# Optimization experiments

Measured on AMD Instinct MI355X. Metric: run time of the kernel, lower is better.

The kernel has to match this reference:

```python
import jax, jax.numpy as jnp
import numpy as np

DIM, H, HD = 512, 8, 64
N_BANK = 4096
EPS = 1e-5


def layernorm(x, g, b):
    m = jnp.mean(x, axis=-1, keepdims=True)
    v = jnp.mean(jnp.square(x - m), axis=-1, keepdims=True)
    return (x - m) * jax.lax.rsqrt(v + EPS) * g + b


def setup_inputs() -> dict:
    key = jax.random.key(0)
    ks = jax.random.split(key, 8)
    # xavier_uniform bound for square (512,512) linears
    bound = float(np.sqrt(6.0 / (DIM + DIM)))
    inp = {
        "x_q": jax.random.normal(ks[0], (32, 128, DIM), jnp.float32),
        "x_k": jax.random.normal(ks[1], (N_BANK, DIM), jnp.float32),
        "x_v": jax.random.normal(ks[2], (N_BANK, DIM), jnp.float32),
        "Wq": jax.random.uniform(ks[3], (DIM, DIM), jnp.float32, -bound, bound),
        "Wk": jax.random.uniform(ks[4], (DIM, DIM), jnp.float32, -bound, bound),
        "Wv": jax.random.uniform(ks[5], (DIM, DIM), jnp.float32, -bound, bound),
        "Wproj": jax.random.uniform(ks[6], (DIM, DIM), jnp.float32, -bound, bound),
        "qn_g": jnp.ones((HD,), jnp.float32),
        "qn_b": jnp.zeros((HD,), jnp.float32),
        "kn_g": jnp.ones((HD,), jnp.float32),
        "kn_b": jnp.zeros((HD,), jnp.float32),
        "n_g": jnp.ones((DIM,), jnp.float32),
        "n_b": jnp.zeros((DIM,), jnp.float32),
    }
    return inp


def reference(x_q, x_k, x_v, Wq, Wk, Wv, Wproj, qn_g, qn_b, kn_g, kn_b, n_g, n_b):
    B, S, D = x_q.shape
    N = x_k.shape[0]
    scale = HD ** (-0.5)
    # Linear layers (torch: y = x @ W.T)
    q = jnp.einsum('bsd,od->bso', x_q, Wq).reshape(B, S, H, HD).transpose(0, 2, 1, 3)  # (B,H,S,hd)
    k = jnp.einsum('nd,od->no', x_k, Wk).reshape(N, H, HD).transpose(1, 0, 2)          # (H,N,hd)
    v = jnp.einsum('nd,od->no', x_v, Wv).reshape(N, H, HD).transpose(1, 0, 2)          # (H,N,hd)
    # per-head qk layernorm
    q = layernorm(q, qn_g, qn_b) * scale
    k = layernorm(k, kn_g, kn_b)
    # cross-attention to shared bank (K/V have no batch dim)
    attn = jnp.einsum('bhsd,hnd->bhsn', q, k)          # (B,H,S,N)
    attn = jax.nn.softmax(attn, axis=-1)
    x = jnp.einsum('bhsn,hnd->bhsd', attn, v)          # (B,H,S,hd)
    x = x.transpose(0, 2, 1, 3).reshape(B, S, D)
    x = layernorm(x, n_g, n_b)
    x = jnp.einsum('bsd,od->bso', x, Wproj)
    return x
```

## Files before the change

### kernel.cpp

```cpp
#include <hip/hip_runtime.h>
#include <hip/hip_bf16.h>
#include <math.h>

#define DIM 512
#define NHEAD 8
#define HD 64
#define NBANK 4096
#define NQROWS 4096
#define EPS 1e-5f
#define QSCALE 0.18033688011f
#define PART_ELEMS (NQROWS * DIM)

typedef __attribute__((ext_vector_type(4))) float floatx4;
typedef __attribute__((ext_vector_type(8))) short short8;

#if defined(__has_builtin)
#if __has_builtin(__builtin_amdgcn_exp2f)
#define EXP2(x) __builtin_amdgcn_exp2f(x)
#endif
#endif
#ifndef EXP2
#define EXP2(x) __expf((x) * 0.69314718056f)
#endif

__device__ __forceinline__ unsigned short f2bf(float f) {
    unsigned int u = __float_as_uint(f);
    u += 0x7fffu + ((u >> 16) & 1u);
    return (unsigned short)(u >> 16);
}
__device__ __forceinline__ float bf2f(unsigned short h) {
    return __uint_as_float(((unsigned int)h) << 16);
}
__device__ __forceinline__ unsigned int pk2(float a, float b) {
    union { __hip_bfloat162 h; unsigned int u; } cvt;
    cvt.h = __float22bfloat162_rn(make_float2(a, b));
    return cvt.u;
}
__device__ __forceinline__ void dma16(const void* gsrc, void* ldst) {
    __builtin_amdgcn_global_load_lds(
        (const __attribute__((address_space(1))) unsigned int*)gsrc,
        (__attribute__((address_space(3))) unsigned int*)ldst, 16, 0, 0);
}

__global__ __launch_bounds__(256) void cvt_kernel(
    const float* __restrict__ Wq, const float* __restrict__ Wk,
    const float* __restrict__ Wv, const float* __restrict__ Wp,
    const float* __restrict__ xq, const float* __restrict__ xk,
    const float* __restrict__ xv,
    unsigned short* __restrict__ Wb, unsigned short* __restrict__ Xb)
{
    const int y = blockIdx.y;
    const float* src;
    unsigned short* dst;
    if (y < 4) {
        if (blockIdx.x >= 128) return;
        src = (y == 0) ? Wq : (y == 1) ? Wk : (y == 2) ? Wv : Wp;
        dst = Wb + (size_t)y * DIM * DIM;
    } else {
        src = (y == 4) ? xq : (y == 5) ? xk : xv;
        dst = Xb + (size_t)(y - 4) * NQROWS * DIM;
    }
    const int i = (blockIdx.x * 256 + threadIdx.x) * 8;
    const int row = i >> 9, kpos = i & 511;
    const int kt = kpos >> 6, seg = (kpos >> 3) & 7;
    const float4 a0 = *(const float4*)(src + i);
    const float4 a1 = *(const float4*)(src + i + 4);
    union { short8 v; unsigned int u[4]; } t;
    t.u[0] = pk2(a0.x, a0.y); t.u[1] = pk2(a0.z, a0.w);
    t.u[2] = pk2(a1.x, a1.y); t.u[3] = pk2(a1.z, a1.w);
    *(short8*)(dst + (size_t)row * 512 + kt * 64 + ((seg ^ (row & 7)) << 3)) = t.v;
}

__global__ __launch_bounds__(256) void qkv_kernel(
    const unsigned short* __restrict__ Xb, const unsigned short* __restrict__ Wb,
    const float* __restrict__ qg, const float* __restrict__ qbeta,
    const float* __restrict__ kg, const float* __restrict__ kbeta,
    unsigned short* __restrict__ Qb, unsigned short* __restrict__ Kb,
    unsigned short* __restrict__ VTb)
{
    __shared__ short8 smem[3072];
    const int tid  = threadIdx.x;
    const int w    = tid >> 6, lane = tid & 63, m = lane & 15, q = lane >> 4;
    const int wr   = w & 1, wc = w >> 1;
    const int row0 = blockIdx.x * 64;
    const int mat  = blockIdx.y >> 2;
    const int col0 = (blockIdx.y & 3) * 128;
    const unsigned short* Xm = Xb + (size_t)mat * NQROWS * DIM;
    const unsigned short* Wm = Wb + (size_t)mat * DIM * DIM;

    const int it0 = tid, it1 = tid + 256;
    const unsigned short* asrc0 = Xm + (size_t)(row0 + (it0 >> 3)) * DIM + (it0 & 7) * 8;
    const unsigned short* asrc1 = Xm + (size_t)(row0 + (it1 >> 3)) * DIM + (it1 & 7) * 8;
    const unsigned short* bsrc[4];
    #pragma unroll
    for (int j = 0; j < 4; ++j) {
        const int item = j * 256 + tid;
        bsrc[j] = Wm + (size_t)(col0 + (item >> 3)) * DIM + (item & 7) * 8;
    }

    floatx4 acc[2][4];
    #pragma unroll
    for (int mt = 0; mt < 2; ++mt)
        #pragma unroll
        for (int nt = 0; nt < 4; ++nt) acc[mt][nt] = (floatx4){0.f, 0.f, 0.f, 0.f};

    {
        short8* as = smem; short8* bs = smem + 512;
        dma16(asrc0, as + w * 64);
        dma16(asrc1, as + 256 + w * 64);
        #pragma unroll
        for (int j = 0; j < 4; ++j)
            dma16(bsrc[j], bs + j * 256 + w * 64);
    }
    __syncthreads();

    for (int kt = 0; kt < 8; ++kt) {
        short8* as = smem + (kt & 1) * 1536;
        short8* bs = as + 512;
        if (kt < 7) {
            short8* asn = smem + ((kt + 1) & 1) * 1536;
            short8* bsn = asn + 512;
            const int o = (kt + 1) * 64;
            dma16(asrc0 + o, asn + w * 64);
            dma16(asrc1 + o, asn + 256 + w * 64);
            #pragma unroll
            for (int j = 0; j < 4; ++j)
                dma16(bsrc[j] + o, bsn + j * 256 + w * 64);
        }
        #pragma unroll
        for (int s = 0; s < 2; ++s) {
            short8 af[2], bfr[4];
            #pragma unroll
            for (int mt = 0; mt < 2; ++mt)
                af[mt] = as[(wr * 32 + mt * 16 + m) * 8 + ((s * 4 + q) ^ (m & 7))];
            #pragma unroll
            for (int nt = 0; nt < 4; ++nt)
                bfr[nt] = bs[(wc * 64 + nt * 16 + m) * 8 + ((s * 4 + q) ^ (m & 7))];
            #pragma unroll
            for (int mt = 0; mt < 2; ++mt)
                #pragma unroll
                for (int nt = 0; nt < 4; ++nt)
                    acc[mt][nt] = __builtin_amdgcn_mfma_f32_16x16x32_bf16(af[mt], bfr[nt], acc[mt][nt], 0, 0, 0);
        }
        __syncthreads();
    }

    if (mat < 2) {
        const float* g = (mat == 0) ? qg : kg;
        const float* be = (mat == 0) ? qbeta : kbeta;
        unsigned short* Y = (mat == 0) ? Qb : Kb;
        float gv[4], bv[4];
        #pragma unroll
        for (int nt = 0; nt < 4; ++nt) { gv[nt] = g[nt * 16 + m]; bv[nt] = be[nt * 16 + m]; }
        #pragma unroll
        for (int mt = 0; mt < 2; ++mt) {
            #pragma unroll
            for (int r = 0; r < 4; ++r) {
                float s = 0.f, sq = 0.f;
                #pragma unroll
                for (int nt = 0; nt < 4; ++nt) { const float v = acc[mt][nt][r]; s += v; sq += v * v; }
                s  += __shfl_xor(s, 1);  s  += __shfl_xor(s, 2);  s  += __shfl_xor(s, 4);  s  += __shfl_xor(s, 8);
                sq += __shfl_xor(sq, 1); sq += __shfl_xor(sq, 2); sq += __shfl_xor(sq, 4); sq += __shfl_xor(sq, 8);
                const float mean = s * (1.f / HD);
                const float var  = sq * (1.f / HD) - mean * mean;
                const float rr   = rsqrtf(var + EPS);
                const int grow = row0 + wr * 32 + mt * 16 + q * 4 + r;
                #pragma unroll
                for (int nt = 0; nt < 4; ++nt) {
                    float v = (acc[mt][nt][r] - mean) * rr * gv[nt] + bv[nt];
                    if (mat == 0) v *= QSCALE;
                    const int col = col0 + wc * 64 + nt * 16 + m;
                    int scol = col;
                    if (mat == 1) {
                        const int o = col & 63, sg2 = o >> 3;
                        scol = (col & ~63) | (((sg2 ^ (grow & 7)) << 3) | (o & 7));
                    }
                    Y[(size_t)grow * DIM + scol] = f2bf(v);
                }
            }
        }
    } else {
        unsigned short* vt = (unsigned short*)smem;
        __syncthreads();
        #pragma unroll
        for (int mt = 0; mt < 2; ++mt)
            #pragma unroll
            for (int nt = 0; nt < 4; ++nt) {
                const int c  = wc * 64 + nt * 16 + m;
                const int rw = wr * 32 + mt * 16 + q * 4;
                *(unsigned int*)(vt + c * 88 + rw)     = pk2(acc[mt][nt][0], acc[mt][nt][1]);
                *(unsigned int*)(vt + c * 88 + rw + 2) = pk2(acc[mt][nt][2], acc[mt][nt][3]);
            }
        __syncthreads();
        #pragma unroll
        for (int p = 0; p < 4; ++p) {
            const int idx = p * 256 + tid;
            const int c = idx >> 3, g = idx & 7;
            const int dglob = col0 + c, hh = dglob >> 6, dl = dglob & 63;
            const int pos = (g >> 2) * 32 + (g & 3) * 4;
            union { short8 v; ushort4 h4[2]; } tv;
            tv.h4[0] = *(const ushort4*)(vt + c * 88 + pos);
            tv.h4[1] = *(const ushort4*)(vt + c * 88 + pos + 16);
            *(short8*)(VTb + ((size_t)(hh * 64 + blockIdx.x) * 512
                              + dl * 8 + (g ^ (dl & 7))) * 8) = tv.v;
        }
    }
}

__global__ __launch_bounds__(256) void attn_kernel(
    const unsigned short* __restrict__ Qb, const unsigned short* __restrict__ Kb,
    const unsigned short* __restrict__ VTb, unsigned short* __restrict__ AOp,
    float* __restrict__ sums)
{
    __shared__ short8 smem[2048];
    const int tid  = threadIdx.x;
    const int w    = tid >> 6;
    const int lane = tid & 63;
    const int m    = lane & 15;
    const int Qd   = lane >> 4;
    const int h    = blockIdx.x & 7;
    const int qgi  = blockIdx.x >> 3;
    const int row0 = qgi * 128;
    const int part = blockIdx.y;
    const int c0   = part * 16;

    const int it0 = tid, it1 = tid + 256;
    const unsigned short* ksrc0 = Kb + (size_t)(it0 >> 3) * DIM + h * HD + (it0 & 7) * 8;
    const unsigned short* ksrc1 = Kb + (size_t)(it1 >> 3) * DIM + h * HD + (it1 & 7) * 8;
    const unsigned short* vbase = VTb + (size_t)h * 64 * 512 * 8;

    short8 qf[2][2];
    #pragma unroll
    for (int mt = 0; mt < 2; ++mt)
        #pragma unroll
        for (int s = 0; s < 2; ++s)
            qf[mt][s] = *(const short8*)(Qb + (size_t)(row0 + w * 32 + mt * 16 + m) * DIM
                                         + h * HD + s * 32 + Qd * 8);

    floatx4 of[4][2];
    floatx4 sacc[2];
    #pragma unroll
    for (int t = 0; t < 4; ++t)
        #pragma unroll
        for (int mt = 0; mt < 2; ++mt) of[t][mt] = (floatx4){0.f, 0.f, 0.f, 0.f};
    #pragma unroll
    for (int mt = 0; mt < 2; ++mt) sacc[mt] = (floatx4){0.f, 0.f, 0.f, 0.f};
    union { short8 v; unsigned int u[4]; } onesu;
    #pragma unroll
    for (int u = 0; u < 4; ++u) onesu.u[u] = 0x3F803F80u;

    {
        short8* ks = smem; short8* vts = smem + 512;
        dma16(ksrc0 + (size_t)c0 * 64 * DIM, ks + w * 64);
        dma16(ksrc1 + (size_t)c0 * 64 * DIM, ks + 256 + w * 64);
        dma16(vbase + ((size_t)c0 * 512 + it0) * 8, vts + w * 64);
        dma16(vbase + ((size_t)c0 * 512 + it1) * 8, vts + 256 + w * 64);
    }
    __syncthreads();

    for (int c = 0; c < 16; ++c) {
        short8* ks  = smem + (c & 1) * 1024;
        short8* vts = ks + 512;
        if (c < 15) {
            short8* ksn  = smem + ((c + 1) & 1) * 1024;
            short8* vtsn = ksn + 512;
            const size_t nc = c0 + c + 1;
            dma16(ksrc0 + nc * 64 * DIM, ksn + w * 64);
            dma16(ksrc1 + nc * 64 * DIM, ksn + 256 + w * 64);
            dma16(vbase + (nc * 512 + it0) * 8, vtsn + w * 64);
            dma16(vbase + (nc * 512 + it1) * 8, vtsn + 256 + w * 64);
        }

        floatx4 st[4][2];
        #pragma unroll
        for (int t = 0; t < 4; ++t)
            #pragma unroll
            for (int mt = 0; mt < 2; ++mt) st[t][mt] = (floatx4){0.f, 0.f, 0.f, 0.f};
        #pragma unroll
        for (int s = 0; s < 2; ++s)
            #pragma unroll
            for (int t = 0; t < 4; ++t) {
                const short8 kf = ks[(t * 16 + m) * 8 + ((s * 4 + Qd) ^ (m & 7))];
                #pragma unroll
                for (int mt = 0; mt < 2; ++mt)
                    st[t][mt] = __builtin_amdgcn_mfma_f32_16x16x32_bf16(kf, qf[mt][s], st[t][mt], 0, 0, 0);
            }

        union { short8 v; unsigned int u[4]; } pf[2][2];
        #pragma unroll
        for (int mt = 0; mt < 2; ++mt)
            #pragma unroll
            for (int s2 = 0; s2 < 2; ++s2)
                #pragma unroll
                for (int u = 0; u < 4; ++u) {
                    const int t = s2 * 2 + (u >> 1), r = (u & 1) * 2;
                    pf[mt][s2].u[u] = pk2(EXP2(st[t][mt][r]), EXP2(st[t][mt][r + 1]));
                }

        #pragma unroll
        for (int mt = 0; mt < 2; ++mt)
            #pragma unroll
            for (int s2 = 0; s2 < 2; ++s2)
                sacc[mt] = __builtin_amdgcn_mfma_f32_16x16x32_bf16(onesu.v, pf[mt][s2].v, sacc[mt], 0, 0, 0);

        #pragma unroll
        for (int s2 = 0; s2 < 2; ++s2)
            #pragma unroll
            for (int t2 = 0; t2 < 4; ++t2) {
                const short8 vf = vts[(t2 * 16 + m) * 8 + ((s2 * 4 + Qd) ^ (m & 7))];
                #pragma unroll
                for (int mt = 0; mt < 2; ++mt)
                    of[t2][mt] = __builtin_amdgcn_mfma_f32_16x16x32_bf16(vf, pf[mt][s2].v, of[t2][mt], 0, 0, 0);
            }
        __syncthreads();
    }

    if (Qd == 0) {
        #pragma unroll
        for (int mt = 0; mt < 2; ++mt)
            sums[((size_t)part * NQROWS + row0 + w * 32 + mt * 16 + m) * NHEAD + h] = sacc[mt][0];
    }

    unsigned int* ob = (unsigned int*)smem;
    #pragma unroll
    for (int t2 = 0; t2 < 4; ++t2)
        #pragma unroll
        for (int mt = 0; mt < 2; ++mt) {
            const int qq  = w * 32 + mt * 16 + m;
            const int blk = t2 * 2 + (Qd >> 1);
            const int sub = (Qd & 1) * 2;
            const int bs  = (blk ^ (qq & 7)) * 4;
            ob[qq * 32 + bs + sub]     = pk2(of[t2][mt][0], of[t2][mt][1]);
            ob[qq * 32 + bs + sub + 1] = pk2(of[t2][mt][2], of[t2][mt][3]);
        }
    __syncthreads();
    #pragma unroll
    for (int pp = 0; pp < 4; ++pp) {
        const int idx = tid + pp * 256;
        const int qq = idx >> 3, sg = idx & 7;
        *(short8*)(AOp + (size_t)part * PART_ELEMS + (size_t)(row0 + qq) * DIM + h * HD + sg * 8) =
            smem[qq * 8 + (sg ^ (qq & 7))];
    }
}

__global__ __launch_bounds__(256) void combine_kernel(
    const unsigned short* __restrict__ AOp, const float* __restrict__ sums,
    const float* __restrict__ g, const float* __restrict__ be,
    unsigned short* __restrict__ AO)
{
    __shared__ float rs[256], rq[256], sm[2], sr[2];
    const int tid  = threadIdx.x;
    const int half = tid >> 7;
    const int row  = blockIdx.x * 2 + half;
    const int t    = tid & 127;
    const int h    = t >> 4;

    float stot = 0.f;
    #pragma unroll
    for (int p = 0; p < 4; ++p)
        stot += sums[((size_t)p * NQROWS + row) * NHEAD + h];

    float o[4] = {0.f, 0.f, 0.f, 0.f};
    #pragma unroll
    for (int p = 0; p < 4; ++p) {
        const ushort4 u = *(const ushort4*)(AOp + (size_t)p * PART_ELEMS + (size_t)row * DIM + t * 4);
        o[0] += bf2f(u.x); o[1] += bf2f(u.y); o[2] += bf2f(u.z); o[3] += bf2f(u.w);
    }
    const float inv = 1.0f / stot;
    const float v0 = o[0] * inv, v1 = o[1] * inv, v2 = o[2] * inv, v3 = o[3] * inv;

    rs[tid] = v0 + v1 + v2 + v3;
    rq[tid] = v0 * v0 + v1 * v1 + v2 * v2 + v3 * v3;
    __syncthreads();
    #pragma unroll
    for (int off = 64; off > 0; off >>= 1) {
        if (t < off) { rs[tid] += rs[tid + off]; rq[tid] += rq[tid + off]; }
        __syncthreads();
    }
    if (t == 0) {
        const float mean = rs[tid] * (1.f / DIM);
        const float var  = rq[tid] * (1.f / DIM) - mean * mean;
        sm[half] = mean;
        sr[half] = rsqrtf(var + EPS);
    }
    __syncthreads();

    const float mean = sm[half], rstd = sr[half];
    const float4 g4 = *(const float4*)(g + t * 4);
    const float4 b4 = *(const float4*)(be + t * 4);
    uint2 packed;
    packed.x = pk2((v0 - mean) * rstd * g4.x + b4.x, (v1 - mean) * rstd * g4.y + b4.y);
    packed.y = pk2((v2 - mean) * rstd * g4.z + b4.z, (v3 - mean) * rstd * g4.w + b4.w);
    const int kt = t >> 4, seg = (t >> 1) & 7, jof = (t & 1) * 4;
    *(uint2*)(AO + (size_t)row * DIM + kt * 64 + ((seg ^ (row & 7)) << 3) + jof) = packed;
}

__global__ __launch_bounds__(256) void final_kernel(
    const unsigned short* __restrict__ AO, const unsigned short* __restrict__ Wpb,
    float* __restrict__ out)
{
    __shared__ short8 fs[2048];
    const int tid  = threadIdx.x;
    const int w    = tid >> 6, lane = tid & 63, m = lane & 15, q = lane >> 4;
    const int row0 = blockIdx.x * 64;
    const int col0 = blockIdx.y * 64;

    const int it0 = tid, it1 = tid + 256;
    const unsigned short* asrc0 = AO  + (size_t)(row0 + (it0 >> 3)) * DIM + (it0 & 7) * 8;
    const unsigned short* asrc1 = AO  + (size_t)(row0 + (it1 >> 3)) * DIM + (it1 & 7) * 8;
    const unsigned short* wsrc0 = Wpb + (size_t)(col0 + (it0 >> 3)) * DIM + (it0 & 7) * 8;
    const unsigned short* wsrc1 = Wpb + (size_t)(col0 + (it1 >> 3)) * DIM + (it1 & 7) * 8;

    floatx4 acc[4];
    #pragma unroll
    for (int mt = 0; mt < 4; ++mt) acc[mt] = (floatx4){0.f, 0.f, 0.f, 0.f};

    {
        dma16(asrc0, fs + w * 64);
        dma16(asrc1, fs + 256 + w * 64);
        dma16(wsrc0, fs + 512 + w * 64);
        dma16(wsrc1, fs + 768 + w * 64);
    }
    __syncthreads();

    for (int kt = 0; kt < 8; ++kt) {
        short8* buf  = fs + (kt & 1) * 1024;
        if (kt < 7) {
            short8* bufn = fs + ((kt + 1) & 1) * 1024;
            const int o = (kt + 1) * 64;
            dma16(asrc0 + o, bufn + w * 64);
            dma16(asrc1 + o, bufn + 256 + w * 64);
            dma16(wsrc0 + o, bufn + 512 + w * 64);
            dma16(wsrc1 + o, bufn + 768 + w * 64);
        }
        #pragma unroll
        for (int s = 0; s < 2; ++s) {
            short8 af[4];
            #pragma unroll
            for (int mt = 0; mt < 4; ++mt)
                af[mt] = buf[(mt * 16 + m) * 8 + ((s * 4 + q) ^ (m & 7))];
            const short8 bfr = buf[512 + (w * 16 + m) * 8 + ((s * 4 + q) ^ (m & 7))];
            #pragma unroll
            for (int mt = 0; mt < 4; ++mt)
                acc[mt] = __builtin_amdgcn_mfma_f32_16x16x32_bf16(af[mt], bfr, acc[mt], 0, 0, 0);
        }
        __syncthreads();
    }

    #pragma unroll
    for (int mt = 0; mt < 4; ++mt)
        #pragma unroll
        for (int r = 0; r < 4; ++r)
            out[(size_t)(row0 + mt * 16 + q * 4 + r) * DIM + col0 + w * 16 + m] = acc[mt][r];
}

extern "C" void kernel_launch(void* const* d_in, const int* in_sizes, int n_in,
                              void* d_out, int out_size, void* d_ws, size_t ws_size,
                              hipStream_t stream)
{
    const float* x_q = (const float*)d_in[0];
    const float* x_k = (const float*)d_in[1];
    const float* x_v = (const float*)d_in[2];
    const float* Wq  = (const float*)d_in[3];
    const float* Wk  = (const float*)d_in[4];
    const float* Wv  = (const float*)d_in[5];
    const float* Wp  = (const float*)d_in[6];
    const float* qg  = (const float*)d_in[7];
    const float* qb  = (const float*)d_in[8];
    const float* kg  = (const float*)d_in[9];
    const float* kb  = (const float*)d_in[10];
    const float* ng  = (const float*)d_in[11];
    const float* nb  = (const float*)d_in[12];
    float* out = (float*)d_out;

    unsigned short* Qb   = (unsigned short*)d_ws;
    unsigned short* Kb   = Qb  + (size_t)NQROWS * DIM;
    unsigned short* VTb  = Kb  + (size_t)NBANK * DIM;
    unsigned short* AOp  = VTb + (size_t)NBANK * DIM;
    float*          sums = (float*)(AOp + (size_t)4 * PART_ELEMS);
    unsigned short* Wb   = (unsigned short*)(sums + (size_t)4 * NQROWS * NHEAD);
    unsigned short* Xb   = AOp;
    unsigned short* AO   = Qb;

    cvt_kernel<<<dim3(1024, 7), 256, 0, stream>>>(Wq, Wk, Wv, Wp, x_q, x_k, x_v, Wb, Xb);
    qkv_kernel<<<dim3(64, 12), 256, 0, stream>>>(Xb, Wb, qg, qb, kg, kb, Qb, Kb, VTb);
    attn_kernel<<<dim3(256, 4), 256, 0, stream>>>(Qb, Kb, VTb, AOp, sums);
    combine_kernel<<<NQROWS / 2, 256, 0, stream>>>(AOp, sums, ng, nb, AO);
    final_kernel<<<dim3(64, 8), 256, 0, stream>>>(AO, Wb + (size_t)3 * DIM * DIM, out);
}
```

Measured before the change: 172.7 us.

## Triple-buffer K/V and GEMM tiles with vmcnt waits; sum softmax in VALU

```diff
diff --git a/kernel.cpp b/kernel.cpp
--- a/kernel.cpp
+++ b/kernel.cpp
@@ -20,7 +20,7 @@
 #endif
 #endif
 #ifndef EXP2
-#define EXP2(x) __expf((x) * 0.69314718056f)
+#define EXP2(x) exp2f(x)
 #endif
 
 __device__ __forceinline__ unsigned short f2bf(float f) {
@@ -212,7 +212,7 @@
     const unsigned short* __restrict__ VTb, unsigned short* __restrict__ AOp,
     float* __restrict__ sums)
 {
-    __shared__ short8 smem[2048];
+    __shared__ short8 smem[3072];
     const int tid  = threadIdx.x;
     const int w    = tid >> 6;
     const int lane = tid & 63;
@@ -238,16 +238,12 @@
                                          + h * HD + s * 32 + Qd * 8);
 
     floatx4 of[4][2];
-    floatx4 sacc[2];
+    float sump[2] = {0.f, 0.f};
     #pragma unroll
     for (int t = 0; t < 4; ++t)
         #pragma unroll
         for (int mt = 0; mt < 2; ++mt) of[t][mt] = (floatx4){0.f, 0.f, 0.f, 0.f};
-    #pragma unroll
-    for (int mt = 0; mt < 2; ++mt) sacc[mt] = (floatx4){0.f, 0.f, 0.f, 0.f};
-    union { short8 v; unsigned int u[4]; } onesu;
-    #pragma unroll
-    for (int u = 0; u < 4; ++u) onesu.u[u] = 0x3F803F80u;
+    const floatx4 fz = (floatx4){0.f, 0.f, 0.f, 0.f};
 
     {
         short8* ks = smem; short8* vts = smem + 512;
@@ -255,16 +251,27 @@
         dma16(ksrc1 + (size_t)c0 * 64 * DIM, ks + 256 + w * 64);
         dma16(vbase + ((size_t)c0 * 512 + it0) * 8, vts + w * 64);
         dma16(vbase + ((size_t)c0 * 512 + it1) * 8, vts + 256 + w * 64);
-    }
-    __syncthreads();
-
+        short8* ks1 = smem + 1024; short8* vts1 = ks1 + 512;
+        const size_t c1 = (size_t)c0 + 1;
+        dma16(ksrc0 + c1 * 64 * DIM, ks1 + w * 64);
+        dma16(ksrc1 + c1 * 64 * DIM, ks1 + 256 + w * 64);
+        dma16(vbase + (c1 * 512 + it0) * 8, vts1 + w * 64);
+        dma16(vbase + (c1 * 512 + it1) * 8, vts1 + 256 + w * 64);
+    }
+
+    int cb = 0, nb = 2;
     for (int c = 0; c < 16; ++c) {
-        short8* ks  = smem + (c & 1) * 1024;
+        if (c < 15) asm volatile("s_waitcnt vmcnt(4)" ::: "memory");
+        else        asm volatile("s_waitcnt vmcnt(0)" ::: "memory");
+        __builtin_amdgcn_s_barrier();
+        __builtin_amdgcn_sched_barrier(0);
+
+        short8* ks  = smem + cb * 1024;
         short8* vts = ks + 512;
-        if (c < 15) {
-            short8* ksn  = smem + ((c + 1) & 1) * 1024;
+        if (c < 14) {
+            short8* ksn  = smem + nb * 1024;
             short8* vtsn = ksn + 512;
-            const size_t nc = c0 + c + 1;
+            const size_t nc = (size_t)(c0 + c + 2);
             dma16(ksrc0 + nc * 64 * DIM, ksn + w * 64);
             dma16(ksrc1 + nc * 64 * DIM, ksn + 256 + w * 64);
             dma16(vbase + (nc * 512 + it0) * 8, vtsn + w * 64);
@@ -273,18 +280,19 @@
 
         floatx4 st[4][2];
         #pragma unroll
-        for (int t = 0; t < 4; ++t)
-            #pragma unroll
-            for (int mt = 0; mt < 2; ++mt) st[t][mt] = (floatx4){0.f, 0.f, 0.f, 0.f};
-        #pragma unroll
-        for (int s = 0; s < 2; ++s)
-            #pragma unroll
-            for (int t = 0; t < 4; ++t) {
-                const short8 kf = ks[(t * 16 + m) * 8 + ((s * 4 + Qd) ^ (m & 7))];
-                #pragma unroll
-                for (int mt = 0; mt < 2; ++mt)
-                    st[t][mt] = __builtin_amdgcn_mfma_f32_16x16x32_bf16(kf, qf[mt][s], st[t][mt], 0, 0, 0);
-            }
+        for (int t = 0; t < 4; ++t) {
+            const short8 kf = ks[(t * 16 + m) * 8 + (Qd ^ (m & 7))];
+            #pragma unroll
+            for (int mt = 0; mt < 2; ++mt)
+                st[t][mt] = __builtin_amdgcn_mfma_f32_16x16x32_bf16(kf, qf[mt][0], fz, 0, 0, 0);
+        }
+        #pragma unroll
+        for (int t = 0; t < 4; ++t) {
+            const short8 kf = ks[(t * 16 + m) * 8 + ((4 + Qd) ^ (m & 7))];
+            #pragma unroll
+            for (int mt = 0; mt < 2; ++mt)
+                st[t][mt] = __builtin_amdgcn_mfma_f32_16x16x32_bf16(kf, qf[mt][1], st[t][mt], 0, 0, 0);
+        }
 
         union { short8 v; unsigned int u[4]; } pf[2][2];
         #pragma unroll
@@ -294,14 +302,12 @@
                 #pragma unroll
                 for (int u = 0; u < 4; ++u) {
                     const int t = s2 * 2 + (u >> 1), r = (u & 1) * 2;
-                    pf[mt][s2].u[u] = pk2(EXP2(st[t][mt][r]), EXP2(st[t][mt][r + 1]));
+                    const float e0 = EXP2(st[t][mt][r]);
+                    const float e1 = EXP2(st[t][mt][r + 1]);
+                    sump[mt] += e0;
+                    sump[mt] += e1;
+                    pf[mt][s2].u[u] = pk2(e0, e1);
                 }
-
-        #pragma unroll
-        for (int mt = 0; mt < 2; ++mt)
-            #pragma unroll
-            for (int s2 = 0; s2 < 2; ++s2)
-                sacc[mt] = __builtin_amdgcn_mfma_f32_16x16x32_bf16(onesu.v, pf[mt][s2].v, sacc[mt], 0, 0, 0);
 
         #pragma unroll
         for (int s2 = 0; s2 < 2; ++s2)
@@ -312,13 +318,23 @@
                 for (int mt = 0; mt < 2; ++mt)
                     of[t2][mt] = __builtin_amdgcn_mfma_f32_16x16x32_bf16(vf, pf[mt][s2].v, of[t2][mt], 0, 0, 0);
             }
-        __syncthreads();
-    }
-
+
+        cb = (cb == 2) ? 0 : cb + 1;
+        nb = (nb == 2) ? 0 : nb + 1;
+    }
+    __syncthreads();
+
+    #pragma unroll
+    for (int mt = 0; mt < 2; ++mt) {
+        float s = sump[mt];
+        s += __shfl_xor(s, 16);
+        s += __shfl_xor(s, 32);
+        sump[mt] = s;
+    }
     if (Qd == 0) {
         #pragma unroll
         for (int mt = 0; mt < 2; ++mt)
-            sums[((size_t)part * NQROWS + row0 + w * 32 + mt * 16 + m) * NHEAD + h] = sacc[mt][0];
+            sums[((size_t)part * NQROWS + row0 + w * 32 + mt * 16 + m) * NHEAD + h] = sump[mt];
     }
 
     unsigned int* ob = (unsigned int*)smem;
@@ -399,7 +415,7 @@
     const unsigned short* __restrict__ AO, const unsigned short* __restrict__ Wpb,
     float* __restrict__ out)
 {
-    __shared__ short8 fs[2048];
+    __shared__ short8 fs[3072];
     const int tid  = threadIdx.x;
     const int w    = tid >> 6, lane = tid & 63, m = lane & 15, q = lane >> 4;
     const int row0 = blockIdx.x * 64;
@@ -420,14 +436,23 @@
         dma16(asrc1, fs + 256 + w * 64);
         dma16(wsrc0, fs + 512 + w * 64);
         dma16(wsrc1, fs + 768 + w * 64);
-    }
-    __syncthreads();
-
+        dma16(asrc0 + 64, fs + 1024 + w * 64);
+        dma16(asrc1 + 64, fs + 1024 + 256 + w * 64);
+        dma16(wsrc0 + 64, fs + 1024 + 512 + w * 64);
+        dma16(wsrc1 + 64, fs + 1024 + 768 + w * 64);
+    }
+
+    int cb = 0, nb = 2;
     for (int kt = 0; kt < 8; ++kt) {
-        short8* buf  = fs + (kt & 1) * 1024;
-        if (kt < 7) {
-            short8* bufn = fs + ((kt + 1) & 1) * 1024;
-            const int o = (kt + 1) * 64;
+        if (kt < 7) asm volatile("s_waitcnt vmcnt(4)" ::: "memory");
+        else        asm volatile("s_waitcnt vmcnt(0)" ::: "memory");
+        __builtin_amdgcn_s_barrier();
+        __builtin_amdgcn_sched_barrier(0);
+
+        short8* buf = fs + cb * 1024;
+        if (kt < 6) {
+            short8* bufn = fs + nb * 1024;
+            const int o = (kt + 2) * 64;
             dma16(asrc0 + o, bufn + w * 64);
             dma16(asrc1 + o, bufn + 256 + w * 64);
             dma16(wsrc0 + o, bufn + 512 + w * 64);
@@ -444,7 +469,8 @@
             for (int mt = 0; mt < 4; ++mt)
                 acc[mt] = __builtin_amdgcn_mfma_f32_16x16x32_bf16(af[mt], bfr, acc[mt], 0, 0, 0);
         }
-        __syncthreads();
+        cb = (cb == 2) ? 0 : cb + 1;
+        nb = (nb == 2) ? 0 : nb + 1;
     }
 
     #pragma unroll
```

Result: faster. 167.2 us (-3.1%).
